# Performance work log

Measured on AMD Instinct MI355X. Metric: run time of the kernel, lower is better.

## Reference

```python
import jax, jax.numpy as jnp
import numpy as np

N, M, D = 4, 512, 1024
H = 16
DK = D // H


def setup_inputs() -> dict:
    rng = jax.random.key(0)
    ks = jax.random.split(rng, 11)
    w = lambda k: jax.random.normal(k, (D, D), jnp.float32) * 0.02
    b = lambda k: jax.random.normal(k, (D,), jnp.float32) * 0.02
    return {
        "query": jax.random.normal(ks[0], (N, M, D), jnp.float32),
        "key": jax.random.normal(ks[1], (N, M, D), jnp.float32),
        "value": jax.random.normal(ks[2], (N, M, D), jnp.float32),
        "Wq": w(ks[3]), "bq": b(ks[4]),
        "Wk": w(ks[5]), "bk": b(ks[6]),
        "Wv": w(ks[7]), "bv": b(ks[8]),
        "Wo": w(ks[9]), "bo": b(ks[10]),
    }


def reference(query, key, value, Wq, bq, Wk, bk, Wv, bv, Wo, bo):
    n, m, d = query.shape
    h, dk = H, d // H
    # torch Linear: y = x @ W.T + b
    q = (query @ Wq.T + bq).reshape(n, m, h, dk)
    k = (key @ Wk.T + bk).reshape(n, m, h, dk)
    v = (value @ Wv.T + bv).reshape(n, m, h, dk)
    # per-token channel outer product: [n,m,h,dk,dk]
    scores = jnp.einsum('nmhd,nmhq->nmhdq', q, k) / np.float32(np.sqrt(dk))
    p_attn = jax.nn.softmax(scores, axis=-1)
    # contract score block with value channels: [n,m,h,dk]
    ctx = jnp.einsum('nmhdq,nmhq->nmhd', p_attn, v).reshape(n, m, d)
    return ctx @ Wo.T + bo
```

## Files before the change

### kernel.cpp

```cpp
#include <hip/hip_runtime.h>
#include <hip/hip_bf16.h>
#include <stdint.h>
#include <stddef.h>

typedef __bf16 bf16_t;
typedef __attribute__((ext_vector_type(8))) __bf16 bf16x8;
typedef __attribute__((ext_vector_type(4))) float f32x4;
typedef __attribute__((ext_vector_type(2))) float f32x2;

#define TOK 2048
#define DMODEL 1024
#define NHEAD 16

__device__ __forceinline__ void gload_lds16(const void* g, void* l) {
  __builtin_amdgcn_global_load_lds(
      (const __attribute__((address_space(1))) void*)g,
      (__attribute__((address_space(3))) void*)l, 16, 0, 0);
}

struct CvtArgs {
  const float* src[7];
  bf16_t* dst[7];
  int n[7];
};

__global__ __launch_bounds__(256) void cvt_kernel(CvtArgs a) {
  int arr = blockIdx.y;
  int n = a.n[arr];
  int i = (blockIdx.x * 256 + threadIdx.x) * 8;
  if (i >= n) return;
  const float* s = a.src[arr];
  bf16_t* d = a.dst[arr];
  f32x4 x0 = *(const f32x4*)(s + i);
  f32x4 x1 = *(const f32x4*)(s + i + 4);
  bf16x8 o;
  o[0] = (bf16_t)x0[0]; o[1] = (bf16_t)x0[1]; o[2] = (bf16_t)x0[2]; o[3] = (bf16_t)x0[3];
  o[4] = (bf16_t)x1[0]; o[5] = (bf16_t)x1[1]; o[6] = (bf16_t)x1[2]; o[7] = (bf16_t)x1[3];
  *(bf16x8*)(d + i) = o;
}

struct GArgs {
  const bf16_t* A[3];
  const bf16_t* W[3];
  const float* bias[3];
  void* C[3];
};

template <bool QKV3, int NJ, typename CT>
__global__ __launch_bounds__(256, 5) void gemmS(GArgs g) {
  constexpr int K = DMODEL, N = DMODEL;
  constexpr int BN = NJ * 32;
  constexpr int nt = K / 64;

  const int i = blockIdx.x;
  const int xcd = i & 7, slot = i >> 3;
  int z, bm, bn;
  if (QKV3) {
    z = slot >> 6;
    const int s = slot & 63;
    bm = (xcd * 4 + (s >> 4)) * 64;
    bn = (s & 15) * 64;
  } else {
    z = 0;
    bm = (xcd * 4 + (slot >> 5)) * 64;
    bn = (slot & 31) * 32;
  }

  const bf16_t* __restrict__ A = g.A[z];
  const bf16_t* __restrict__ W = g.W[z];
  const float* __restrict__ bias = g.bias[z];
  CT* __restrict__ C = (CT*)g.C[z];

  __shared__ alignas(16) bf16_t As[2][64 * 64];
  __shared__ alignas(16) bf16_t Bs[2][BN * 64];

  const int tid = threadIdx.x;
  const int wv = tid >> 6, lane = tid & 63;
  const int wr = (wv >> 1) * 32;
  const int wc = (wv & 1) * (16 * NJ);
  const int lm = lane & 15, lch = lane >> 4;
  const int cr4 = (lane >> 4) * 4;

  const int sr8 = lane >> 3;
  const int sc = (lane & 7) ^ sr8;
  const bf16_t* Asrc = A + (size_t)(bm + wv * 16 + sr8) * K + sc * 8;
  const bf16_t* Wsrc = W + (size_t)(bn + wv * 8 * NJ + sr8) * K + sc * 8;

  f32x4 acc[2][NJ] = {};

#define STAGE(T)                                                               \
  {                                                                            \
    const int _b = (T) & 1;                                                    \
    _Pragma("unroll") for (int j = 0; j < 2; ++j)                              \
        gload_lds16(Asrc + (size_t)(j * 8) * K + (T) * 64,                     \
                    &As[_b][(wv * 16 + j * 8) * 64]);                          \
    _Pragma("unroll") for (int j = 0; j < NJ; ++j)                             \
        gload_lds16(Wsrc + (size_t)(j * 8) * K + (T) * 64,                     \
                    &Bs[_b][(wv * 8 * NJ + j * 8) * 64]);                      \
  }

  STAGE(0);

#pragma unroll 1
  for (int T = 0; T < nt; ++T) {
    __syncthreads();
    if (T + 1 < nt) STAGE(T + 1);
    __builtin_amdgcn_sched_barrier(0);

    const int b = T & 1;
#pragma unroll
    for (int kk = 0; kk < 2; ++kk) {
      bf16x8 fa[2], fb[NJ];
#pragma unroll
      for (int ii = 0; ii < 2; ++ii) {
        const int ra = wr + ii * 16 + lm;
        fa[ii] = *(const bf16x8*)&As[b][ra * 64 + (((kk * 4 + lch) ^ (ra & 7)) * 8)];
      }
#pragma unroll
      for (int jj = 0; jj < NJ; ++jj) {
        const int rb = wc + jj * 16 + lm;
        fb[jj] = *(const bf16x8*)&Bs[b][rb * 64 + (((kk * 4 + lch) ^ (rb & 7)) * 8)];
      }
#pragma unroll
      for (int ii = 0; ii < 2; ++ii)
#pragma unroll
        for (int jj = 0; jj < NJ; ++jj)
          acc[ii][jj] = __builtin_amdgcn_mfma_f32_16x16x32_bf16(
              fa[ii], fb[jj], acc[ii][jj], 0, 0, 0);
    }
  }
#undef STAGE

#pragma unroll
  for (int ii = 0; ii < 2; ++ii)
#pragma unroll
    for (int jj = 0; jj < NJ; ++jj) {
      const int col = bn + wc + jj * 16 + lm;
      const float bvv = bias[col];
#pragma unroll
      for (int r = 0; r < 4; ++r) {
        const int row = bm + wr + ii * 16 + cr4 + r;
        C[(size_t)row * N + col] = (CT)(acc[ii][jj][r] + bvv);
      }
    }
}

__global__ __launch_bounds__(256) void attn_kernel(
    const bf16_t* __restrict__ q, const bf16_t* __restrict__ k,
    const bf16_t* __restrict__ v, bf16_t* __restrict__ ctx) {
  __shared__ float kS[4][64];
  __shared__ float vS[4][64];
  const int wv = threadIdx.x >> 6, lane = threadIdx.x & 63;
  const int pair = blockIdx.x * 4 + wv;
  const size_t base = (size_t)pair * 64;
  const float sc = 0.125f * 1.44269504088896341f;
  const float qd = (float)q[base + lane];
  kS[wv][lane] = (float)k[base + lane];
  vS[wv][lane] = (float)v[base + lane];
  asm volatile("s_waitcnt lgkmcnt(0)" ::: "memory");
  const float a = qd * sc;
  const f32x2 av = {a, a};
  f32x2 sum = {0.f, 0.f}, acc = {0.f, 0.f};
#pragma unroll
  for (int j = 0; j < 64; j += 4) {
    f32x4 k4 = *(const f32x4*)&kS[wv][j];
    f32x4 v4 = *(const f32x4*)&vS[wv][j];
    f32x2 t0 = av * (f32x2){k4[0], k4[1]};
    f32x2 t1 = av * (f32x2){k4[2], k4[3]};
    f32x2 e0 = {__builtin_amdgcn_exp2f(t0[0]), __builtin_amdgcn_exp2f(t0[1])};
    f32x2 e1 = {__builtin_amdgcn_exp2f(t1[0]), __builtin_amdgcn_exp2f(t1[1])};
    sum += e0 + e1;
    acc += e0 * (f32x2){v4[0], v4[1]} + e1 * (f32x2){v4[2], v4[3]};
  }
  const float s = sum[0] + sum[1];
  const float o = acc[0] + acc[1];
  ctx[base + lane] = (bf16_t)(o * __builtin_amdgcn_rcpf(s));
}

extern "C" void kernel_launch(void* const* d_in, const int* in_sizes, int n_in,
                              void* d_out, int out_size, void* d_ws, size_t ws_size,
                              hipStream_t stream) {
  const float* query = (const float*)d_in[0];
  const float* key   = (const float*)d_in[1];
  const float* value = (const float*)d_in[2];
  const float* Wq = (const float*)d_in[3];
  const float* bq = (const float*)d_in[4];
  const float* Wk = (const float*)d_in[5];
  const float* bk = (const float*)d_in[6];
  const float* Wv = (const float*)d_in[7];
  const float* bv = (const float*)d_in[8];
  const float* Wo = (const float*)d_in[9];
  const float* bo = (const float*)d_in[10];
  float* out = (float*)d_out;

  const size_t XE = (size_t)TOK * DMODEL;
  const size_t WE = (size_t)DMODEL * DMODEL;

  char* ws = (char*)d_ws;
  size_t off = 0;
  bf16_t* xb[3];
  for (int i = 0; i < 3; ++i) { xb[i] = (bf16_t*)(ws + off); off += XE * 2; }
  bf16_t* wb[4];
  for (int i = 0; i < 4; ++i) { wb[i] = (bf16_t*)(ws + off); off += WE * 2; }
  bf16_t* pb[3];
  for (int i = 0; i < 3; ++i) { pb[i] = (bf16_t*)(ws + off); off += XE * 2; }
  bf16_t* ctxb = (bf16_t*)(ws + off); off += XE * 2;

  CvtArgs ca;
  ca.src[0] = query; ca.src[1] = key; ca.src[2] = value;
  ca.src[3] = Wq; ca.src[4] = Wk; ca.src[5] = Wv; ca.src[6] = Wo;
  ca.dst[0] = xb[0]; ca.dst[1] = xb[1]; ca.dst[2] = xb[2];
  ca.dst[3] = wb[0]; ca.dst[4] = wb[1]; ca.dst[5] = wb[2]; ca.dst[6] = wb[3];
  ca.n[0] = ca.n[1] = ca.n[2] = (int)XE;
  ca.n[3] = ca.n[4] = ca.n[5] = ca.n[6] = (int)WE;
  cvt_kernel<<<dim3((unsigned)(XE / (256 * 8)), 7), 256, 0, stream>>>(ca);

  GArgs g1;
  g1.A[0] = xb[0]; g1.A[1] = xb[1]; g1.A[2] = xb[2];
  g1.W[0] = wb[0]; g1.W[1] = wb[1]; g1.W[2] = wb[2];
  g1.bias[0] = bq; g1.bias[1] = bk; g1.bias[2] = bv;
  g1.C[0] = pb[0]; g1.C[1] = pb[1]; g1.C[2] = pb[2];
  gemmS<true, 2, bf16_t><<<dim3(1536), 256, 0, stream>>>(g1);

  attn_kernel<<<dim3(TOK * NHEAD / 4), 256, 0, stream>>>(pb[0], pb[1], pb[2], ctxb);

  GArgs g2;
  g2.A[0] = ctxb; g2.W[0] = wb[3]; g2.bias[0] = bo; g2.C[0] = out;
  g2.A[1] = ctxb; g2.W[1] = wb[3]; g2.bias[1] = bo; g2.C[1] = out;
  g2.A[2] = ctxb; g2.W[2] = wb[3]; g2.bias[2] = bo; g2.C[2] = out;
  gemmS<false, 1, float><<<dim3(1024), 256, 0, stream>>>(g2);
}
```

Measured before the change: 68.62 us.

## Fuse activation fp32-to-bf16 conversion into QKV GEMM A-tile loading

The QKV projection GEMM now reads fp32 activations directly through registers, converts them to bf16 and writes them into swizzled LDS, prefetching two tiles ahead. The separate conversion pass for query/key/value and their bf16 workspace buffers are removed, so only the weights are converted up front. This saves a full write and read of the bf16 activation copies. In exchange, each GEMM block reads twice as many bytes for A, and the loads go through VGPRs instead of direct-to-LDS, which adds register pressure.

```diff
diff --git a/kernel.cpp b/kernel.cpp
--- a/kernel.cpp
+++ b/kernel.cpp
@@ -19,16 +19,13 @@
 }
 
 struct CvtArgs {
-  const float* src[7];
-  bf16_t* dst[7];
-  int n[7];
+  const float* src[4];
+  bf16_t* dst[4];
 };
 
 __global__ __launch_bounds__(256) void cvt_kernel(CvtArgs a) {
   int arr = blockIdx.y;
-  int n = a.n[arr];
   int i = (blockIdx.x * 256 + threadIdx.x) * 8;
-  if (i >= n) return;
   const float* s = a.src[arr];
   bf16_t* d = a.dst[arr];
   f32x4 x0 = *(const f32x4*)(s + i);
@@ -40,16 +37,15 @@
 }
 
 struct GArgs {
-  const bf16_t* A[3];
+  const void* A[3];
   const bf16_t* W[3];
   const float* bias[3];
   void* C[3];
 };
 
-template <bool QKV3, int NJ, typename CT>
+template <bool AF32, bool QKV3, int NJ, typename CT>
 __global__ __launch_bounds__(256, 5) void gemmS(GArgs g) {
   constexpr int K = DMODEL, N = DMODEL;
-  constexpr int BN = NJ * 32;
   constexpr int nt = K / 64;
 
   const int i = blockIdx.x;
@@ -66,13 +62,12 @@
     bn = (slot & 31) * 32;
   }
 
-  const bf16_t* __restrict__ A = g.A[z];
   const bf16_t* __restrict__ W = g.W[z];
   const float* __restrict__ bias = g.bias[z];
   CT* __restrict__ C = (CT*)g.C[z];
 
   __shared__ alignas(16) bf16_t As[2][64 * 64];
-  __shared__ alignas(16) bf16_t Bs[2][BN * 64];
+  __shared__ alignas(16) bf16_t Bs[2][NJ * 32 * 64];
 
   const int tid = threadIdx.x;
   const int wv = tid >> 6, lane = tid & 63;
@@ -83,28 +78,70 @@
 
   const int sr8 = lane >> 3;
   const int sc = (lane & 7) ^ sr8;
-  const bf16_t* Asrc = A + (size_t)(bm + wv * 16 + sr8) * K + sc * 8;
   const bf16_t* Wsrc = W + (size_t)(bn + wv * 8 * NJ + sr8) * K + sc * 8;
+  const bf16_t* Asrc = AF32 ? nullptr
+                            : ((const bf16_t*)g.A[z] + (size_t)(bm + wv * 16 + sr8) * K + sc * 8);
+
+  const int trow = tid >> 2;
+  const int c0 = (tid & 3) * 2;
+  const float* Af = AF32 ? ((const float*)g.A[z] + (size_t)(bm + trow) * K + c0 * 8) : nullptr;
+  const int aw0 = trow * 64 + ((c0 ^ (trow & 7)) * 8);
+  const int aw1 = trow * 64 + (((c0 + 1) ^ (trow & 7)) * 8);
 
   f32x4 acc[2][NJ] = {};
-
-#define STAGE(T)                                                               \
+  f32x4 hA[4];
+
+#define STAGE_W(T)                                                             \
+  _Pragma("unroll") for (int j = 0; j < NJ; ++j)                               \
+      gload_lds16(Wsrc + (size_t)(j * 8) * K + (T) * 64,                       \
+                  &Bs[(T) & 1][(wv * 8 * NJ + j * 8) * 64]);
+
+#define STAGE_A(T)                                                             \
+  _Pragma("unroll") for (int j = 0; j < 2; ++j)                                \
+      gload_lds16(Asrc + (size_t)(j * 8) * K + (T) * 64,                       \
+                  &As[(T) & 1][(wv * 16 + j * 8) * 64]);
+
+#define LOADA(T)                                                               \
   {                                                                            \
-    const int _b = (T) & 1;                                                    \
-    _Pragma("unroll") for (int j = 0; j < 2; ++j)                              \
-        gload_lds16(Asrc + (size_t)(j * 8) * K + (T) * 64,                     \
-                    &As[_b][(wv * 16 + j * 8) * 64]);                          \
-    _Pragma("unroll") for (int j = 0; j < NJ; ++j)                             \
-        gload_lds16(Wsrc + (size_t)(j * 8) * K + (T) * 64,                     \
-                    &Bs[_b][(wv * 8 * NJ + j * 8) * 64]);                      \
-  }
-
-  STAGE(0);
+    const float* _p = Af + (T) * 64;                                           \
+    hA[0] = *(const f32x4*)(_p);      hA[1] = *(const f32x4*)(_p + 4);         \
+    hA[2] = *(const f32x4*)(_p + 8);  hA[3] = *(const f32x4*)(_p + 12);        \
+  }
+
+#define WRITEA(T)                                                              \
+  {                                                                            \
+    bf16x8 _c0, _c1;                                                           \
+    _Pragma("unroll") for (int e = 0; e < 4; ++e) {                            \
+      _c0[e] = (bf16_t)hA[0][e]; _c0[e + 4] = (bf16_t)hA[1][e];                \
+      _c1[e] = (bf16_t)hA[2][e]; _c1[e + 4] = (bf16_t)hA[3][e];                \
+    }                                                                          \
+    *(bf16x8*)&As[(T) & 1][aw0] = _c0;                                         \
+    *(bf16x8*)&As[(T) & 1][aw1] = _c1;                                         \
+  }
+
+  if (AF32) {
+    STAGE_W(0);
+    LOADA(0);
+    asm volatile("s_waitcnt vmcnt(0)" ::: "memory");
+    WRITEA(0);
+    LOADA(1);
+  } else {
+    STAGE_A(0);
+    STAGE_W(0);
+  }
 
 #pragma unroll 1
   for (int T = 0; T < nt; ++T) {
     __syncthreads();
-    if (T + 1 < nt) STAGE(T + 1);
+    if (T + 1 < nt) {
+      STAGE_W(T + 1);
+      if (AF32) {
+        WRITEA(T + 1);
+      } else {
+        STAGE_A(T + 1);
+      }
+    }
+    if (AF32 && T + 2 < nt) LOADA(T + 2);
     __builtin_amdgcn_sched_barrier(0);
 
     const int b = T & 1;
@@ -129,7 +166,10 @@
               fa[ii], fb[jj], acc[ii][jj], 0, 0, 0);
     }
   }
-#undef STAGE
+#undef STAGE_W
+#undef STAGE_A
+#undef LOADA
+#undef WRITEA
 
 #pragma unroll
   for (int ii = 0; ii < 2; ++ii)
@@ -198,8 +238,6 @@
 
   char* ws = (char*)d_ws;
   size_t off = 0;
-  bf16_t* xb[3];
-  for (int i = 0; i < 3; ++i) { xb[i] = (bf16_t*)(ws + off); off += XE * 2; }
   bf16_t* wb[4];
   for (int i = 0; i < 4; ++i) { wb[i] = (bf16_t*)(ws + off); off += WE * 2; }
   bf16_t* pb[3];
@@ -207,20 +245,16 @@
   bf16_t* ctxb = (bf16_t*)(ws + off); off += XE * 2;
 
   CvtArgs ca;
-  ca.src[0] = query; ca.src[1] = key; ca.src[2] = value;
-  ca.src[3] = Wq; ca.src[4] = Wk; ca.src[5] = Wv; ca.src[6] = Wo;
-  ca.dst[0] = xb[0]; ca.dst[1] = xb[1]; ca.dst[2] = xb[2];
-  ca.dst[3] = wb[0]; ca.dst[4] = wb[1]; ca.dst[5] = wb[2]; ca.dst[6] = wb[3];
-  ca.n[0] = ca.n[1] = ca.n[2] = (int)XE;
-  ca.n[3] = ca.n[4] = ca.n[5] = ca.n[6] = (int)WE;
-  cvt_kernel<<<dim3((unsigned)(XE / (256 * 8)), 7), 256, 0, stream>>>(ca);
+  ca.src[0] = Wq; ca.src[1] = Wk; ca.src[2] = Wv; ca.src[3] = Wo;
+  ca.dst[0] = wb[0]; ca.dst[1] = wb[1]; ca.dst[2] = wb[2]; ca.dst[3] = wb[3];
+  cvt_kernel<<<dim3((unsigned)(WE / (256 * 8)), 4), 256, 0, stream>>>(ca);
 
   GArgs g1;
-  g1.A[0] = xb[0]; g1.A[1] = xb[1]; g1.A[2] = xb[2];
+  g1.A[0] = query; g1.A[1] = key; g1.A[2] = value;
   g1.W[0] = wb[0]; g1.W[1] = wb[1]; g1.W[2] = wb[2];
   g1.bias[0] = bq; g1.bias[1] = bk; g1.bias[2] = bv;
   g1.C[0] = pb[0]; g1.C[1] = pb[1]; g1.C[2] = pb[2];
-  gemmS<true, 2, bf16_t><<<dim3(1536), 256, 0, stream>>>(g1);
+  gemmS<true, true, 2, bf16_t><<<dim3(1536), 256, 0, stream>>>(g1);
 
   attn_kernel<<<dim3(TOK * NHEAD / 4), 256, 0, stream>>>(pb[0], pb[1], pb[2], ctxb);
 
@@ -228,5 +262,5 @@
   g2.A[0] = ctxb; g2.W[0] = wb[3]; g2.bias[0] = bo; g2.C[0] = out;
   g2.A[1] = ctxb; g2.W[1] = wb[3]; g2.bias[1] = bo; g2.C[1] = out;
   g2.A[2] = ctxb; g2.W[2] = wb[3]; g2.bias[2] = bo; g2.C[2] = out;
-  gemmS<false, 1, float><<<dim3(1024), 256, 0, stream>>>(g2);
-}
+  gemmS<false, false, 1, float><<<dim3(1024), 256, 0, stream>>>(g2);
+}
```

Result: slower. 75.45 us (+9.9%).
